# Optimization experiments

Measured on AMD Instinct MI355X. Metric: run time of the kernel, lower is better.

The kernel has to match this reference:

```python
import jax, jax.numpy as jnp
import numpy as np

N_NODES = 50000
N_REL = 8
N_EDGES = 100000
IN_SIZE = 128
OUT_SIZE = 128


def setup_inputs() -> dict:
    key = jax.random.key(0)
    k1, k2, k3, k4, k5 = jax.random.split(key, 5)
    inp = jax.random.normal(k1, (N_NODES, IN_SIZE), dtype=jnp.float32)
    src = jax.random.randint(k2, (N_REL, N_EDGES), 0, N_NODES, dtype=jnp.int32)
    dst = jax.random.randint(k3, (N_REL, N_EDGES), 0, N_NODES, dtype=jnp.int32)
    vals = jax.random.uniform(k4, (N_REL, N_EDGES), dtype=jnp.float32)
    weights = jax.random.normal(k5, (N_REL, IN_SIZE, OUT_SIZE), dtype=jnp.float32) * (1.0 / np.sqrt(IN_SIZE))
    return {"inp": inp, "src": src, "dst": dst, "vals": vals, "weights": weights}


def reference(inp, src, dst, vals, weights):
    # Per-relation sparse adj @ inp:  agg[r] = A_r @ inp, A_r given as COO edges.
    n_nodes = inp.shape[0]

    def rel_agg(s, d, v):
        msgs = v[:, None] * inp[s]                      # [E, in]
        return jax.ops.segment_sum(msgs, d, num_segments=n_nodes)  # [N, in]

    agg = jax.vmap(rel_agg)(src, dst, vals)             # [R, N, in]
    # concat along features then block-stacked weight matmul == per-relation
    # matmul summed over relations: out = sum_r agg[r] @ W[r]
    out = jnp.einsum('rni,rio->no', agg, weights)       # [N, out]
    return out
```

## Files before the change

kernel.cpp:

```cpp
#include <hip/hip_runtime.h>


constexpr int IN  = 128;
constexpr int OUT = 128;
constexpr int LDK = 136;
constexpr int NPB = 64;
constexpr int LDA = 132;
constexpr int CAPMAX = 256;
constexpr int NBINS_MAX = 1024;
constexpr int EPB = 8192;

typedef __attribute__((ext_vector_type(8))) short bf16x8;
typedef __attribute__((ext_vector_type(4))) float f32x4;

__device__ inline unsigned short f2bf(float f) {
    unsigned int u = __float_as_uint(f);
    u += 0x7fffu + ((u >> 16) & 1u);
    return (unsigned short)(u >> 16);
}
__device__ inline float bflo(unsigned int u) { return __uint_as_float(u << 16); }
__device__ inline float bfhi(unsigned int u) { return __uint_as_float(u & 0xffff0000u); }
__device__ inline unsigned int pack2bf(float a, float b) {
    return (unsigned)f2bf(a) | ((unsigned)f2bf(b) << 16);
}

__global__ __launch_bounds__(256) void conv_inp_kernel(
    const float* __restrict__ x, unsigned short* __restrict__ y, int n8)
{
    const int i = blockIdx.x * 256 + threadIdx.x;
    if (i >= n8) return;
    const float4 a = ((const float4*)x)[i * 2];
    const float4 b = ((const float4*)x)[i * 2 + 1];
    uint4 o;
    o.x = pack2bf(a.x, a.y);
    o.y = pack2bf(a.z, a.w);
    o.z = pack2bf(b.x, b.y);
    o.w = pack2bf(b.z, b.w);
    ((uint4*)y)[i] = o;
}

__global__ __launch_bounds__(256) void conv_w_kernel(
    const float* __restrict__ w, unsigned short* __restrict__ wt, int total)
{
    const int t = blockIdx.x * 256 + threadIdx.x;
    if (t >= total) return;
    const int r = t >> 14, rem = t & 16383;
    const int n = rem >> 7, k = rem & 127;
    wt[t] = f2bf(w[(r << 14) + (k << 7) + n]);
}

__global__ __launch_bounds__(256) void prep_kernel(
    const float* __restrict__ x, unsigned short* __restrict__ y, int n8, int nbI,
    const float* __restrict__ w, unsigned short* __restrict__ wtb, int wtot, int nbW,
    const int* __restrict__ src, const int* __restrict__ dst,
    const float* __restrict__ vals, int* __restrict__ bin_cnt,
    int2* __restrict__ binned, int4* __restrict__ spill,
    int* __restrict__ spill_cnt,
    int n_edges, int n_nodes, int nbins, int cap, int spill_max, int fgx)
{
    __shared__ int hist[NBINS_MAX];
    __shared__ int gbase[NBINS_MAX];

    const int bid = blockIdx.x;
    const int tid = threadIdx.x;
    if (bid < nbI) {
        const int i = bid * 256 + tid;
        if (i >= n8) return;
        const float4 a = ((const float4*)x)[i * 2];
        const float4 b = ((const float4*)x)[i * 2 + 1];
        uint4 o;
        o.x = pack2bf(a.x, a.y);
        o.y = pack2bf(a.z, a.w);
        o.z = pack2bf(b.x, b.y);
        o.w = pack2bf(b.z, b.w);
        ((uint4*)y)[i] = o;
        return;
    }
    if (bid < nbI + nbW) {
        const int t = (bid - nbI) * 256 + tid;
        if (t >= wtot) return;
        const int r = t >> 14, rem = t & 16383;
        const int n = rem >> 7, k = rem & 127;
        wtb[t] = f2bf(w[(r << 14) + (k << 7) + n]);
        return;
    }
    const int idx = bid - nbI - nbW;
    const int rel = idx / fgx;
    const int e0 = (idx - rel * fgx) * EPB;
    const size_t gbase_e = (size_t)rel * n_edges;

    for (int b = tid; b < nbins; b += 256) hist[b] = 0;
    __syncthreads();

    for (int j = 0; j < EPB / 256; ++j) {
        const int e = e0 + j * 256 + tid;
        if (e < n_edges) atomicAdd(&hist[dst[gbase_e + e] >> 6], 1);
    }
    __syncthreads();

    for (int b = tid; b < nbins; b += 256) {
        const int c = hist[b];
        gbase[b] = c ? atomicAdd(&bin_cnt[rel * nbins + b], c) : 0;
        hist[b] = 0;
    }
    __syncthreads();

    for (int j = 0; j < EPB / 256; ++j) {
        const int e = e0 + j * 256 + tid;
        if (e >= n_edges) continue;
        const int d = dst[gbase_e + e];
        const int s = src[gbase_e + e];
        const float v = vals[gbase_e + e];
        const int b = d >> 6;
        const int lp = atomicAdd(&hist[b], 1);
        const int pos = gbase[b] + lp;
        if (pos < cap) {
            binned[(size_t)(rel * nbins + b) * cap + pos] =
                make_int2(((d & 63) << 19) | s, __float_as_int(v));
        } else {
            const int sp = atomicAdd(spill_cnt, 1);
            if (sp < spill_max)
                spill[sp] = make_int4(d, (rel << 19) | s, __float_as_int(v), 0);
        }
    }
}

__global__ __launch_bounds__(256, 4) void bin_gemm_kernel(
    const unsigned short* __restrict__ inpb,
    const unsigned short* __restrict__ wt,
    const int2* __restrict__ binned, const int* __restrict__ bin_cnt,
    float* __restrict__ out, int n_nodes, int nbins, int cap, int n_rel)
{
    __shared__ float A[NPB * LDA];
    __shared__ int2 sorted[CAPMAX];
    __shared__ int lcnt[NPB], loff[NPB + 1], lcur[NPB];

    const int bin = blockIdx.x;
    const int tid = threadIdx.x;
    const int wave = tid >> 6, lane = tid & 63;
    const int m = lane & 15, q = lane >> 4;

    f32x4 acc[4][2];
    #pragma unroll
    for (int mt = 0; mt < 4; ++mt) {
        acc[mt][0] = (f32x4){0.f, 0.f, 0.f, 0.f};
        acc[mt][1] = (f32x4){0.f, 0.f, 0.f, 0.f};
    }

    for (int r = 0; r < n_rel; ++r) {
        const int2* __restrict__ cellp =
            binned + (size_t)(r * nbins + bin) * cap;
        int cnt = bin_cnt[r * nbins + bin];
        if (cnt > cap) cnt = cap;

        __syncthreads();
        {
            float* zp = &A[(tid >> 2) * LDA + (tid & 3) * 32];
            #pragma unroll
            for (int i = 0; i < 8; ++i)
                *(float4*)(zp + i * 4) = make_float4(0.f, 0.f, 0.f, 0.f);
        }
        if (tid < NPB) { lcnt[tid] = 0; lcur[tid] = 0; }
        __syncthreads();

        for (int i = tid; i < cnt; i += 256)
            atomicAdd(&lcnt[(cellp[i].x >> 19) & 63], 1);
        __syncthreads();

        if (tid < 64) {
            const int v = lcnt[tid];
            int incl = v;
            #pragma unroll
            for (int off = 1; off < 64; off <<= 1) {
                const int t = __shfl_up(incl, off, 64);
                if (tid >= off) incl += t;
            }
            loff[tid] = incl - v;
            if (tid == 63) loff[64] = incl;
        }
        __syncthreads();

        for (int i = tid; i < cnt; i += 256) {
            const int2 e = cellp[i];
            const int g = (e.x >> 19) & 63;
            const int pos = atomicAdd(&lcur[g], 1);
            sorted[loff[g] + pos] = e;
        }
        __syncthreads();

        {
            const int g0 = wave * 16;
            const int start = loff[g0];
            const int end = loff[g0 + 16];
            int cur = g0;
            float a0 = 0.f, a1 = 0.f;
            int i = start;
            for (; i + 8 <= end; i += 8) {
                int2 e[8]; unsigned int u[8];
                #pragma unroll
                for (int k = 0; k < 8; ++k) e[k] = sorted[i + k];
                #pragma unroll
                for (int k = 0; k < 8; ++k)
                    u[k] = ((const unsigned int*)(
                        inpb + (size_t)(e[k].x & 0x7ffff) * IN))[lane];
                #pragma unroll
                for (int k = 0; k < 8; ++k) {
                    const int ln = (e[k].x >> 19) & 63;
                    if (ln != cur) {
                        *(float2*)&A[cur * LDA + lane * 2] =
                            make_float2(a0, a1);
                        a0 = 0.f; a1 = 0.f; cur = ln;
                    }
                    const float v = __int_as_float(e[k].y);
                    a0 += v * bflo(u[k]); a1 += v * bfhi(u[k]);
                }
            }
            for (; i < end; ++i) {
                const int2 e1 = sorted[i];
                const unsigned int u1 = ((const unsigned int*)(
                    inpb + (size_t)(e1.x & 0x7ffff) * IN))[lane];
                const int ln = (e1.x >> 19) & 63;
                if (ln != cur) {
                    *(float2*)&A[cur * LDA + lane * 2] = make_float2(a0, a1);
                    a0 = 0.f; a1 = 0.f; cur = ln;
                }
                const float v = __int_as_float(e1.y);
                a0 += v * bflo(u1); a1 += v * bfhi(u1);
            }
            *(float2*)&A[cur * LDA + lane * 2] = make_float2(a0, a1);
        }
        __syncthreads();

        const unsigned short* wtr = wt + ((size_t)r * OUT + wave * 32) * IN;
        bf16x8 bfrag[2][4];
        #pragma unroll
        for (int nt = 0; nt < 2; ++nt)
            #pragma unroll
            for (int ks = 0; ks < 4; ++ks)
                bfrag[nt][ks] = *(const bf16x8*)(
                    wtr + (size_t)(nt * 16 + m) * IN + ks * 32 + q * 8);

        #pragma unroll
        for (int ks = 0; ks < 4; ++ks) {
            bf16x8 a[4];
            #pragma unroll
            for (int mt = 0; mt < 4; ++mt) {
                const float* Ap = &A[(mt * 16 + m) * LDA + ks * 32 + q * 8];
                const float4 lo = *(const float4*)Ap;
                const float4 hi = *(const float4*)(Ap + 4);
                union { uint4 u; bf16x8 v; } cv;
                cv.u = make_uint4(pack2bf(lo.x, lo.y), pack2bf(lo.z, lo.w),
                                  pack2bf(hi.x, hi.y), pack2bf(hi.z, hi.w));
                a[mt] = cv.v;
            }
            #pragma unroll
            for (int mt = 0; mt < 4; ++mt) {
                acc[mt][0] = __builtin_amdgcn_mfma_f32_16x16x32_bf16(
                    a[mt], bfrag[0][ks], acc[mt][0], 0, 0, 0);
                acc[mt][1] = __builtin_amdgcn_mfma_f32_16x16x32_bf16(
                    a[mt], bfrag[1][ks], acc[mt][1], 0, 0, 0);
            }
        }
    }

    const int row0 = bin * NPB;
    #pragma unroll
    for (int mt = 0; mt < 4; ++mt) {
        #pragma unroll
        for (int rg = 0; rg < 4; ++rg) {
            const int row = row0 + mt * 16 + q * 4 + rg;
            if (row < n_nodes) {
                float* op = out + (size_t)row * OUT + wave * 32 + m;
                op[0]  = acc[mt][0][rg];
                op[16] = acc[mt][1][rg];
            }
        }
    }
}

__global__ __launch_bounds__(256) void spill_w_kernel(
    const unsigned short* __restrict__ inpb,
    const unsigned short* __restrict__ wt,
    const int4* __restrict__ spill, const int* __restrict__ spill_cnt,
    float* __restrict__ out, int spill_max)
{
    int n = *spill_cnt;
    if (n > spill_max) n = spill_max;
    const int w = (blockIdx.x * 256 + threadIdx.x) >> 6;
    const int lane = threadIdx.x & 63;
    const int nw = gridDim.x * 4;
    for (int i = w; i < n; i += nw) {
        const int4 s = spill[i];
        const int d = s.x;
        const int rel = s.y >> 19, srcrow = s.y & 0x7ffff;
        const float v = __int_as_float(s.z);
        const unsigned short* irow = inpb + (size_t)srcrow * IN;
        #pragma unroll
        for (int cc = 0; cc < 2; ++cc) {
            const int col = lane * 2 + cc;
            const unsigned short* wrow = wt + ((size_t)rel * OUT + col) * IN;
            float acc = 0.f;
            for (int k8 = 0; k8 < IN; k8 += 8) {
                const uint4 iw = *(const uint4*)(irow + k8);
                const uint4 ww = *(const uint4*)(wrow + k8);
                acc += bflo(iw.x)*bflo(ww.x) + bfhi(iw.x)*bfhi(ww.x)
                     + bflo(iw.y)*bflo(ww.y) + bfhi(iw.y)*bfhi(ww.y)
                     + bflo(iw.z)*bflo(ww.z) + bfhi(iw.z)*bfhi(ww.z)
                     + bflo(iw.w)*bflo(ww.w) + bfhi(iw.w)*bfhi(ww.w);
            }
            __hip_atomic_fetch_add(out + (size_t)d * OUT + col, v * acc,
                                   __ATOMIC_RELAXED, __HIP_MEMORY_SCOPE_AGENT);
        }
    }
}

__global__ __launch_bounds__(256) void mfma_gemm(
    const unsigned short* __restrict__ inpb,
    const unsigned short* __restrict__ wt,
    unsigned short* __restrict__ h, int rel_base, int n_nodes)
{
    __shared__ unsigned short As[128 * LDK];

    const int rel = rel_base + blockIdx.y;
    const int row0 = blockIdx.x * 128;
    const int tid = threadIdx.x;
    const int wave = tid >> 6, lane = tid & 63;
    const int m = lane & 15, q = lane >> 4;

    {
        const int r = tid >> 1;
        const int half = (tid & 1) * 64;
        const int grow = row0 + r;
        const uint4* gp = (const uint4*)(inpb + (size_t)grow * IN + half);
        uint4* lp = (uint4*)&As[r * LDK + half];
        #pragma unroll
        for (int i = 0; i < 8; ++i) {
            uint4 v = make_uint4(0u, 0u, 0u, 0u);
            if (grow < n_nodes) v = gp[i];
            lp[i] = v;
        }
    }

    bf16x8 bfrag[2][4];
    {
        const unsigned short* wtr = wt + ((size_t)rel * OUT + wave * 32) * IN;
        #pragma unroll
        for (int nt = 0; nt < 2; ++nt)
            #pragma unroll
            for (int ks = 0; ks < 4; ++ks)
                bfrag[nt][ks] = *(const bf16x8*)(
                    wtr + (size_t)(nt * 16 + m) * IN + ks * 32 + q * 8);
    }

    __syncthreads();

    f32x4 acc[8][2];
    #pragma unroll
    for (int mt = 0; mt < 8; ++mt)
        #pragma unroll
        for (int nt = 0; nt < 2; ++nt)
            acc[mt][nt] = (f32x4){0.f, 0.f, 0.f, 0.f};

    #pragma unroll
    for (int ks = 0; ks < 4; ++ks) {
        bf16x8 a[8];
        #pragma unroll
        for (int mt = 0; mt < 8; ++mt)
            a[mt] = *(const bf16x8*)&As[(mt * 16 + m) * LDK + ks * 32 + q * 8];
        #pragma unroll
        for (int mt = 0; mt < 8; ++mt) {
            acc[mt][0] = __builtin_amdgcn_mfma_f32_16x16x32_bf16(
                a[mt], bfrag[0][ks], acc[mt][0], 0, 0, 0);
            acc[mt][1] = __builtin_amdgcn_mfma_f32_16x16x32_bf16(
                a[mt], bfrag[1][ks], acc[mt][1], 0, 0, 0);
        }
    }

    unsigned short* hrel = h + (size_t)blockIdx.y * n_nodes * OUT;
    #pragma unroll
    for (int mt = 0; mt < 8; ++mt) {
        #pragma unroll
        for (int rg = 0; rg < 4; ++rg) {
            const int row = row0 + mt * 16 + q * 4 + rg;
            if (row < n_nodes) {
                unsigned short* hp = hrel + (size_t)row * OUT + wave * 32 + m;
                hp[0]  = f2bf(acc[mt][0][rg]);
                hp[16] = f2bf(acc[mt][1][rg]);
            }
        }
    }
}

__global__ __launch_bounds__(256) void fill_kernel(
    const int* __restrict__ src, const int* __restrict__ dst,
    const float* __restrict__ vals, int* __restrict__ counts,
    int2* __restrict__ bucket, int4* __restrict__ spill,
    int* __restrict__ spill_cnt, int n_edges, int n_nodes,
    int cap, int spill_max)
{
    const int e = blockIdx.x * 256 + threadIdx.x;
    if (e >= n_edges) return;
    const size_t g = (size_t)blockIdx.y * n_edges + e;
    const int d = dst[g];
    const int enc = blockIdx.y * n_nodes + src[g];
    const int pos = atomicAdd(&counts[d], 1);
    if (pos < cap) {
        bucket[(size_t)d * cap + pos] = make_int2(enc, __float_as_int(vals[g]));
    } else {
        const int sp = atomicAdd(spill_cnt, 1);
        if (sp < spill_max)
            spill[sp] = make_int4(d, enc, __float_as_int(vals[g]), 0);
    }
}

__global__ __launch_bounds__(256) void gather_kernel(
    const unsigned short* __restrict__ h, const int2* __restrict__ bucket,
    const int* __restrict__ counts, float* __restrict__ out,
    int n_nodes, int cap, int accum)
{
    const int node = blockIdx.x * 8 + (threadIdx.x >> 5);
    const int lane = threadIdx.x & 31;
    if (node >= n_nodes) return;
    int cnt = counts[node];
    if (cnt > cap) cnt = cap;
    const int2* __restrict__ b = bucket + (size_t)node * cap;
    float4* __restrict__ op = (float4*)(out + (size_t)node * OUT);

    float4 acc = accum ? op[lane] : make_float4(0.f, 0.f, 0.f, 0.f);
    int j = 0;
    for (; j + 4 <= cnt; j += 4) {
        const int2 r0 = b[j], r1 = b[j + 1], r2 = b[j + 2], r3 = b[j + 3];
        const uint2 h0 = ((const uint2*)(h + (size_t)r0.x * OUT))[lane];
        const uint2 h1 = ((const uint2*)(h + (size_t)r1.x * OUT))[lane];
        const uint2 h2 = ((const uint2*)(h + (size_t)r2.x * OUT))[lane];
        const uint2 h3 = ((const uint2*)(h + (size_t)r3.x * OUT))[lane];
        const float v0 = __int_as_float(r0.y), v1 = __int_as_float(r1.y);
        const float v2 = __int_as_float(r2.y), v3 = __int_as_float(r3.y);
        acc.x += v0*bflo(h0.x) + v1*bflo(h1.x) + v2*bflo(h2.x) + v3*bflo(h3.x);
        acc.y += v0*bfhi(h0.x) + v1*bfhi(h1.x) + v2*bfhi(h2.x) + v3*bfhi(h3.x);
        acc.z += v0*bflo(h0.y) + v1*bflo(h1.y) + v2*bflo(h2.y) + v3*bflo(h3.y);
        acc.w += v0*bfhi(h0.y) + v1*bfhi(h1.y) + v2*bfhi(h2.y) + v3*bfhi(h3.y);
    }
    for (; j < cnt; ++j) {
        const int2 r0 = b[j];
        const float v = __int_as_float(r0.y);
        const uint2 hv = ((const uint2*)(h + (size_t)r0.x * OUT))[lane];
        acc.x += v * bflo(hv.x); acc.y += v * bfhi(hv.x);
        acc.z += v * bflo(hv.y); acc.w += v * bfhi(hv.y);
    }
    op[lane] = acc;
}

__global__ __launch_bounds__(256) void spill_kernel(
    const unsigned short* __restrict__ h, const int4* __restrict__ spill,
    const int* __restrict__ spill_cnt, float* __restrict__ out, int spill_max)
{
    int n = *spill_cnt;
    if (n > spill_max) n = spill_max;
    const int w = (blockIdx.x * 256 + threadIdx.x) >> 6;
    const int lane = threadIdx.x & 63;
    const int nw = gridDim.x * 4;
    for (int i = w; i < n; i += nw) {
        const int4 s = spill[i];
        const float v = __int_as_float(s.z);
        const unsigned int u = ((const unsigned int*)(h + (size_t)s.y * OUT))[lane];
        float* __restrict__ orow = out + (size_t)s.x * OUT;
        __hip_atomic_fetch_add(orow + lane * 2,     v * bflo(u),
                               __ATOMIC_RELAXED, __HIP_MEMORY_SCOPE_AGENT);
        __hip_atomic_fetch_add(orow + lane * 2 + 1, v * bfhi(u),
                               __ATOMIC_RELAXED, __HIP_MEMORY_SCOPE_AGENT);
    }
}

__global__ __launch_bounds__(256) void scatter_kernel(
    const unsigned short* __restrict__ h, const int* __restrict__ src,
    const int* __restrict__ dst, const float* __restrict__ vals,
    float* __restrict__ out, int n_edges)
{
    const int e = blockIdx.x * 8 + (threadIdx.x >> 5);
    if (e >= n_edges) return;
    const int lane = threadIdx.x & 31;
    const int s = src[e];
    const int d = dst[e];
    const float v = vals[e];
    const unsigned int* __restrict__ hrow =
        (const unsigned int*)(h + (size_t)s * OUT);
    float* __restrict__ orow = out + (size_t)d * OUT;
    #pragma unroll
    for (int kk = 0; kk < 2; ++kk) {
        const int jj = lane + kk * 32;
        const unsigned int u = hrow[jj];
        __hip_atomic_fetch_add(orow + jj * 2,     v * bflo(u),
                               __ATOMIC_RELAXED, __HIP_MEMORY_SCOPE_AGENT);
        __hip_atomic_fetch_add(orow + jj * 2 + 1, v * bfhi(u),
                               __ATOMIC_RELAXED, __HIP_MEMORY_SCOPE_AGENT);
    }
}

extern "C" void kernel_launch(void* const* d_in, const int* in_sizes, int n_in,
                              void* d_out, int out_size, void* d_ws, size_t ws_size,
                              hipStream_t stream) {
    const float* inp     = (const float*)d_in[0];
    const int*   src     = (const int*)  d_in[1];
    const int*   dst     = (const int*)  d_in[2];
    const float* vals    = (const float*)d_in[3];
    const float* weights = (const float*)d_in[4];
    float* out = (float*)d_out;

    const int n_nodes = in_sizes[0] / IN;
    const int n_rel   = in_sizes[4] / (IN * OUT);
    const int n_edges = in_sizes[1] / n_rel;

    auto align_up = [](size_t x) { return (x + 255) & ~(size_t)255; };
    const int SPILL_MAX = 65536;
    const size_t sz_inpb   = align_up((size_t)n_nodes * IN * 2);
    const size_t sz_wt     = align_up((size_t)n_rel * IN * OUT * 2);
    const size_t sz_spill  = align_up((size_t)SPILL_MAX * 16);

    const int conv_n8 = n_nodes * IN / 8;
    const int wt_tot  = n_rel * IN * OUT;
    const int gemm_gx = (n_nodes + 127) / 128;
    const int gath_gx = (n_nodes + 7) / 8;
    const int fill_gx = (n_edges + 255) / 256;
    const int nbins   = (n_nodes + NPB - 1) / NPB;

    if (n_rel <= 8 && n_nodes < (1 << 19) && nbins <= NBINS_MAX) {
        const size_t ncells  = (size_t)n_rel * nbins;
        const size_t sz_bcnt = align_up((ncells + 1) * 4);
        int cap = 0;
        const int caps[] = {256, 192, 128};
        for (int c : caps) {
            const size_t sz_binned = align_up(ncells * c * 8);
            if (sz_inpb + sz_wt + sz_bcnt + sz_spill + sz_binned <= ws_size) {
                cap = c; break;
            }
        }
        if (cap > 0) {
            const size_t sz_binned = align_up(ncells * cap * 8);
            char* p = (char*)d_ws;
            unsigned short* inpb = (unsigned short*)p;  p += sz_inpb;
            unsigned short* wtb  = (unsigned short*)p;  p += sz_wt;
            int*   bin_cnt = (int*)p;   p += sz_bcnt;
            int4*  spill   = (int4*)p;  p += sz_spill;
            int2*  binned  = (int2*)p;  p += sz_binned;
            int*   spill_cnt = bin_cnt + ncells;

            const int nbI = (conv_n8 + 255) / 256;
            const int nbW = (wt_tot + 255) / 256;
            const int fgx = (n_edges + EPB - 1) / EPB;
            const int nF  = fgx * n_rel;

            hipMemsetAsync(bin_cnt, 0, (ncells + 1) * 4, stream);
            prep_kernel<<<nbI + nbW + nF, 256, 0, stream>>>(
                inp, inpb, conv_n8, nbI, weights, wtb, wt_tot, nbW,
                src, dst, vals, bin_cnt, binned, spill, spill_cnt,
                n_edges, n_nodes, nbins, cap, SPILL_MAX, fgx);
            bin_gemm_kernel<<<nbins, 256, 0, stream>>>(
                inpb, wtb, binned, bin_cnt, out, n_nodes, nbins, cap, n_rel);
            spill_w_kernel<<<128, 256, 0, stream>>>(
                inpb, wtb, spill, spill_cnt, out, SPILL_MAX);
            return;
        }
    }

    const size_t sz_counts = align_up((size_t)(n_nodes + 1) * 4);
    const size_t fixed = sz_inpb + sz_wt + sz_counts + sz_spill;

    {
        const size_t sz_h = (size_t)n_rel * n_nodes * OUT * 2;
        int cap = 0;
        const int caps[] = {64, 48, 32, 24, 20};
        for (int c : caps) {
            if (fixed + sz_h + align_up((size_t)n_nodes * c * 8) <= ws_size) {
                cap = c; break;
            }
        }
        if (cap > 0) {
            char* p = (char*)d_ws;
            unsigned short* inpb = (unsigned short*)p;  p += sz_inpb;
            unsigned short* wtb  = (unsigned short*)p;  p += sz_wt;
            int*   counts = (int*)p;    p += sz_counts;
            int4*  spill  = (int4*)p;   p += sz_spill;
            unsigned short* h = (unsigned short*)p;     p += sz_h;
            int2*  bucket = (int2*)p;
            int*   spill_cnt = counts + n_nodes;

            conv_inp_kernel<<<(conv_n8 + 255) / 256, 256, 0, stream>>>(
                inp, inpb, conv_n8);
            conv_w_kernel<<<(wt_tot + 255) / 256, 256, 0, stream>>>(
                weights, wtb, wt_tot);
            hipMemsetAsync(counts, 0, (size_t)(n_nodes + 1) * 4, stream);
            dim3 fg(fill_gx, n_rel);
            fill_kernel<<<fg, 256, 0, stream>>>(src, dst, vals, counts, bucket,
                                                spill, spill_cnt, n_edges,
                                                n_nodes, cap, SPILL_MAX);
            dim3 gg(gemm_gx, n_rel);
            mfma_gemm<<<gg, 256, 0, stream>>>(inpb, wtb, h, 0, n_nodes);
            gather_kernel<<<gath_gx, 256, 0, stream>>>(h, bucket, counts, out,
                                                       n_nodes, cap, 0);
            spill_kernel<<<128, 256, 0, stream>>>(h, spill, spill_cnt, out,
                                                  SPILL_MAX);
            return;
        }
    }

    {
        char* p = (char*)d_ws;
        unsigned short* inpb = (unsigned short*)p;  p += sz_inpb;
        unsigned short* wtb  = (unsigned short*)p;  p += sz_wt;
        unsigned short* h = (unsigned short*)p;

        conv_inp_kernel<<<(conv_n8 + 255) / 256, 256, 0, stream>>>(
            inp, inpb, conv_n8);
        conv_w_kernel<<<(wt_tot + 255) / 256, 256, 0, stream>>>(
            weights, wtb, wt_tot);
        hipMemsetAsync(out, 0, (size_t)n_nodes * OUT * 4, stream);
        const int sgx = (n_edges + 7) / 8;
        for (int r = 0; r < n_rel; ++r) {
            const size_t eoff = (size_t)r * n_edges;
            dim3 gg(gemm_gx, 1);
            mfma_gemm<<<gg, 256, 0, stream>>>(inpb, wtb, h, r, n_nodes);
            scatter_kernel<<<sgx, 256, 0, stream>>>(h, src + eoff, dst + eoff,
                                                    vals + eoff, out, n_edges);
        }
    }
}
```

Measured before the change: 226.5 us.

## Halve node bins to 32 rows, prefetch next relation's edges, split prep kernel

Shrinks the per-block node tile from 64 to 32 rows, which doubles the number of bins and blocks and raises the occupancy hint to 6. Each thread now holds at most one edge register-resident per relation and prefetches the next relation's edge during the gather, removing the per-relation global reloads of the bin. The fused prep kernel is split into a conversion kernel and a separate binning kernel, the bin capacity options are lowered, and the scalar tail loop is replaced by a padded 8-wide loop. Smaller tiles mean less work per block to amortize the weight loads across the MFMA stage, and a lower capacity may push more edges into the spill path.

```diff
diff --git a/kernel.cpp b/kernel.cpp
--- a/kernel.cpp
+++ b/kernel.cpp
@@ -4,10 +4,10 @@
 constexpr int IN  = 128;
 constexpr int OUT = 128;
 constexpr int LDK = 136;
-constexpr int NPB = 64;
+constexpr int NPB = 32;
 constexpr int LDA = 132;
-constexpr int CAPMAX = 256;
-constexpr int NBINS_MAX = 1024;
+constexpr int CAPMAX = 192;
+constexpr int NBINS_MAX = 2048;
 constexpr int EPB = 8192;
 
 typedef __attribute__((ext_vector_type(8))) short bf16x8;
@@ -49,22 +49,13 @@
     wt[t] = f2bf(w[(r << 14) + (k << 7) + n]);
 }
 
-__global__ __launch_bounds__(256) void prep_kernel(
-    const float* __restrict__ x, unsigned short* __restrict__ y, int n8, int nbI,
-    const float* __restrict__ w, unsigned short* __restrict__ wtb, int wtot, int nbW,
-    const int* __restrict__ src, const int* __restrict__ dst,
-    const float* __restrict__ vals, int* __restrict__ bin_cnt,
-    int2* __restrict__ binned, int4* __restrict__ spill,
-    int* __restrict__ spill_cnt,
-    int n_edges, int n_nodes, int nbins, int cap, int spill_max, int fgx)
-{
-    __shared__ int hist[NBINS_MAX];
-    __shared__ int gbase[NBINS_MAX];
-
-    const int bid = blockIdx.x;
-    const int tid = threadIdx.x;
-    if (bid < nbI) {
-        const int i = bid * 256 + tid;
+__global__ __launch_bounds__(256) void conv_both_kernel(
+    const float* __restrict__ x, unsigned short* __restrict__ y, int n8,
+    const float* __restrict__ w, unsigned short* __restrict__ wt, int total,
+    int nb_inp)
+{
+    if (blockIdx.x < nb_inp) {
+        const int i = blockIdx.x * 256 + threadIdx.x;
         if (i >= n8) return;
         const float4 a = ((const float4*)x)[i * 2];
         const float4 b = ((const float4*)x)[i * 2 + 1];
@@ -74,27 +65,36 @@
         o.z = pack2bf(b.x, b.y);
         o.w = pack2bf(b.z, b.w);
         ((uint4*)y)[i] = o;
-        return;
-    }
-    if (bid < nbI + nbW) {
-        const int t = (bid - nbI) * 256 + tid;
-        if (t >= wtot) return;
+    } else {
+        const int t = (blockIdx.x - nb_inp) * 256 + threadIdx.x;
+        if (t >= total) return;
         const int r = t >> 14, rem = t & 16383;
         const int n = rem >> 7, k = rem & 127;
-        wtb[t] = f2bf(w[(r << 14) + (k << 7) + n]);
-        return;
-    }
-    const int idx = bid - nbI - nbW;
-    const int rel = idx / fgx;
-    const int e0 = (idx - rel * fgx) * EPB;
-    const size_t gbase_e = (size_t)rel * n_edges;
+        wt[t] = f2bf(w[(r << 14) + (k << 7) + n]);
+    }
+}
+
+__global__ __launch_bounds__(256) void fill2_kernel(
+    const int* __restrict__ src, const int* __restrict__ dst,
+    const float* __restrict__ vals, int* __restrict__ bin_cnt,
+    int2* __restrict__ binned, int4* __restrict__ spill,
+    int* __restrict__ spill_cnt,
+    int n_edges, int n_nodes, int nbins, int cap, int spill_max, int fgx)
+{
+    __shared__ int hist[NBINS_MAX];
+    __shared__ int gbase[NBINS_MAX];
+
+    const int tid = threadIdx.x;
+    const int rel = blockIdx.x / fgx;
+    const int e0 = (blockIdx.x - rel * fgx) * EPB;
+    const size_t base_e = (size_t)rel * n_edges;
 
     for (int b = tid; b < nbins; b += 256) hist[b] = 0;
     __syncthreads();
 
     for (int j = 0; j < EPB / 256; ++j) {
         const int e = e0 + j * 256 + tid;
-        if (e < n_edges) atomicAdd(&hist[dst[gbase_e + e] >> 6], 1);
+        if (e < n_edges) atomicAdd(&hist[dst[base_e + e] >> 5], 1);
     }
     __syncthreads();
 
@@ -108,15 +108,15 @@
     for (int j = 0; j < EPB / 256; ++j) {
         const int e = e0 + j * 256 + tid;
         if (e >= n_edges) continue;
-        const int d = dst[gbase_e + e];
-        const int s = src[gbase_e + e];
-        const float v = vals[gbase_e + e];
-        const int b = d >> 6;
+        const int d = dst[base_e + e];
+        const int s = src[base_e + e];
+        const float v = vals[base_e + e];
+        const int b = d >> 5;
         const int lp = atomicAdd(&hist[b], 1);
         const int pos = gbase[b] + lp;
         if (pos < cap) {
             binned[(size_t)(rel * nbins + b) * cap + pos] =
-                make_int2(((d & 63) << 19) | s, __float_as_int(v));
+                make_int2(((d & 31) << 19) | s, __float_as_int(v));
         } else {
             const int sp = atomicAdd(spill_cnt, 1);
             if (sp < spill_max)
@@ -125,7 +125,7 @@
     }
 }
 
-__global__ __launch_bounds__(256, 4) void bin_gemm_kernel(
+__global__ __launch_bounds__(256, 6) void bin_gemm_kernel(
     const unsigned short* __restrict__ inpb,
     const unsigned short* __restrict__ wt,
     const int2* __restrict__ binned, const int* __restrict__ bin_cnt,
@@ -133,79 +133,96 @@
 {
     __shared__ float A[NPB * LDA];
     __shared__ int2 sorted[CAPMAX];
-    __shared__ int lcnt[NPB], loff[NPB + 1], lcur[NPB];
+    __shared__ int lcnt[NPB];
+    __shared__ int loff[NPB + 1];
+    __shared__ int lcur[NPB];
+    __shared__ int relcnt[8];
 
     const int bin = blockIdx.x;
     const int tid = threadIdx.x;
     const int wave = tid >> 6, lane = tid & 63;
     const int m = lane & 15, q = lane >> 4;
 
-    f32x4 acc[4][2];
+    if (tid < n_rel) {
+        int c = bin_cnt[tid * nbins + bin];
+        relcnt[tid] = c > cap ? cap : c;
+    }
+    if (tid < NPB) { lcnt[tid] = 0; lcur[tid] = 0; }
+    __syncthreads();
+
+    int2 ecur = make_int2((NPB - 1) << 19, 0);
+    if (tid < relcnt[0])
+        ecur = binned[(size_t)bin * cap + tid];
+
+    f32x4 acc[2][2];
     #pragma unroll
-    for (int mt = 0; mt < 4; ++mt) {
+    for (int mt = 0; mt < 2; ++mt) {
         acc[mt][0] = (f32x4){0.f, 0.f, 0.f, 0.f};
         acc[mt][1] = (f32x4){0.f, 0.f, 0.f, 0.f};
     }
 
     for (int r = 0; r < n_rel; ++r) {
-        const int2* __restrict__ cellp =
-            binned + (size_t)(r * nbins + bin) * cap;
-        int cnt = bin_cnt[r * nbins + bin];
-        if (cnt > cap) cnt = cap;
-
+        const int cnt = relcnt[r];
+
+        {
+            float4* A4 = (float4*)A;
+            #pragma unroll
+            for (int j = 0; j < (NPB * LDA / 4 + 255) / 256; ++j) {
+                const int idx = j * 256 + tid;
+                if (idx < NPB * LDA / 4)
+                    A4[idx] = make_float4(0.f, 0.f, 0.f, 0.f);
+            }
+        }
+        if (tid < cnt) atomicAdd(&lcnt[(ecur.x >> 19) & (NPB - 1)], 1);
         __syncthreads();
-        {
-            float* zp = &A[(tid >> 2) * LDA + (tid & 3) * 32];
-            #pragma unroll
-            for (int i = 0; i < 8; ++i)
-                *(float4*)(zp + i * 4) = make_float4(0.f, 0.f, 0.f, 0.f);
-        }
-        if (tid < NPB) { lcnt[tid] = 0; lcur[tid] = 0; }
-        __syncthreads();
-
-        for (int i = tid; i < cnt; i += 256)
-            atomicAdd(&lcnt[(cellp[i].x >> 19) & 63], 1);
-        __syncthreads();
-
-        if (tid < 64) {
+
+        if (tid < NPB) {
             const int v = lcnt[tid];
             int incl = v;
             #pragma unroll
-            for (int off = 1; off < 64; off <<= 1) {
-                const int t = __shfl_up(incl, off, 64);
+            for (int off = 1; off < NPB; off <<= 1) {
+                const int t = __shfl_up(incl, off, NPB);
                 if (tid >= off) incl += t;
             }
             loff[tid] = incl - v;
-            if (tid == 63) loff[64] = incl;
+            if (tid == NPB - 1) loff[NPB] = incl;
         }
         __syncthreads();
 
-        for (int i = tid; i < cnt; i += 256) {
-            const int2 e = cellp[i];
-            const int g = (e.x >> 19) & 63;
+        if (tid < cnt) {
+            const int g = (ecur.x >> 19) & (NPB - 1);
             const int pos = atomicAdd(&lcur[g], 1);
-            sorted[loff[g] + pos] = e;
-        }
+            sorted[loff[g] + pos] = ecur;
+        }
+        if (tid < NPB) lcnt[tid] = 0;
         __syncthreads();
 
+        int2 enext = make_int2((NPB - 1) << 19, 0);
+        if (r + 1 < n_rel && tid < relcnt[r + 1])
+            enext = binned[(size_t)((r + 1) * nbins + bin) * cap + tid];
+
         {
-            const int g0 = wave * 16;
+            const int g0 = wave * 8;
+            const int gend = g0 + 7;
             const int start = loff[g0];
-            const int end = loff[g0 + 16];
+            const int end = loff[g0 + 8];
             int cur = g0;
             float a0 = 0.f, a1 = 0.f;
-            int i = start;
-            for (; i + 8 <= end; i += 8) {
+            for (int i = start; i < end; i += 8) {
                 int2 e[8]; unsigned int u[8];
                 #pragma unroll
-                for (int k = 0; k < 8; ++k) e[k] = sorted[i + k];
+                for (int k = 0; k < 8; ++k) {
+                    const int idx = i + k;
+                    e[k] = (idx < end) ? sorted[idx]
+                                       : make_int2(gend << 19, 0);
+                }
                 #pragma unroll
                 for (int k = 0; k < 8; ++k)
                     u[k] = ((const unsigned int*)(
                         inpb + (size_t)(e[k].x & 0x7ffff) * IN))[lane];
                 #pragma unroll
                 for (int k = 0; k < 8; ++k) {
-                    const int ln = (e[k].x >> 19) & 63;
+                    const int ln = (e[k].x >> 19) & (NPB - 1);
                     if (ln != cur) {
                         *(float2*)&A[cur * LDA + lane * 2] =
                             make_float2(a0, a1);
@@ -215,20 +232,9 @@
                     a0 += v * bflo(u[k]); a1 += v * bfhi(u[k]);
                 }
             }
-            for (; i < end; ++i) {
-                const int2 e1 = sorted[i];
-                const unsigned int u1 = ((const unsigned int*)(
-                    inpb + (size_t)(e1.x & 0x7ffff) * IN))[lane];
-                const int ln = (e1.x >> 19) & 63;
-                if (ln != cur) {
-                    *(float2*)&A[cur * LDA + lane * 2] = make_float2(a0, a1);
-                    a0 = 0.f; a1 = 0.f; cur = ln;
-                }
-                const float v = __int_as_float(e1.y);
-                a0 += v * bflo(u1); a1 += v * bfhi(u1);
-            }
             *(float2*)&A[cur * LDA + lane * 2] = make_float2(a0, a1);
         }
+        if (tid < NPB) lcur[tid] = 0;
         __syncthreads();
 
         const unsigned short* wtr = wt + ((size_t)r * OUT + wave * 32) * IN;
@@ -242,9 +248,9 @@
 
         #pragma unroll
         for (int ks = 0; ks < 4; ++ks) {
-            bf16x8 a[4];
+            bf16x8 a[2];
             #pragma unroll
-            for (int mt = 0; mt < 4; ++mt) {
+            for (int mt = 0; mt < 2; ++mt) {
                 const float* Ap = &A[(mt * 16 + m) * LDA + ks * 32 + q * 8];
                 const float4 lo = *(const float4*)Ap;
                 const float4 hi = *(const float4*)(Ap + 4);
@@ -254,18 +260,20 @@
                 a[mt] = cv.v;
             }
             #pragma unroll
-            for (int mt = 0; mt < 4; ++mt) {
+            for (int mt = 0; mt < 2; ++mt) {
                 acc[mt][0] = __builtin_amdgcn_mfma_f32_16x16x32_bf16(
                     a[mt], bfrag[0][ks], acc[mt][0], 0, 0, 0);
                 acc[mt][1] = __builtin_amdgcn_mfma_f32_16x16x32_bf16(
                     a[mt], bfrag[1][ks], acc[mt][1], 0, 0, 0);
             }
         }
+        ecur = enext;
+        __syncthreads();
     }
 
     const int row0 = bin * NPB;
     #pragma unroll
-    for (int mt = 0; mt < 4; ++mt) {
+    for (int mt = 0; mt < 2; ++mt) {
         #pragma unroll
         for (int rg = 0; rg < 4; ++rg) {
             const int row = row0 + mt * 16 + q * 4 + rg;
@@ -528,7 +536,7 @@
         const size_t ncells  = (size_t)n_rel * nbins;
         const size_t sz_bcnt = align_up((ncells + 1) * 4);
         int cap = 0;
-        const int caps[] = {256, 192, 128};
+        const int caps[] = {192, 160, 128};
         for (int c : caps) {
             const size_t sz_binned = align_up(ncells * c * 8);
             if (sz_inpb + sz_wt + sz_bcnt + sz_spill + sz_binned <= ws_size) {
@@ -548,11 +556,11 @@
             const int nbI = (conv_n8 + 255) / 256;
             const int nbW = (wt_tot + 255) / 256;
             const int fgx = (n_edges + EPB - 1) / EPB;
-            const int nF  = fgx * n_rel;
 
             hipMemsetAsync(bin_cnt, 0, (ncells + 1) * 4, stream);
-            prep_kernel<<<nbI + nbW + nF, 256, 0, stream>>>(
-                inp, inpb, conv_n8, nbI, weights, wtb, wt_tot, nbW,
+            conv_both_kernel<<<nbI + nbW, 256, 0, stream>>>(
+                inp, inpb, conv_n8, weights, wtb, wt_tot, nbI);
+            fill2_kernel<<<fgx * n_rel, 256, 0, stream>>>(
                 src, dst, vals, bin_cnt, binned, spill, spill_cnt,
                 n_edges, n_nodes, nbins, cap, SPILL_MAX, fgx);
             bin_gemm_kernel<<<nbins, 256, 0, stream>>>(
```

Result: slower. 267.0 us (+17.9%).
